# Kernel tuning notes

Hardware: AMD Instinct MI355X
Metric: run time of the kernel (lower is better)

The kernel has to match this reference:

```python
import jax, jax.numpy as jnp
import numpy as np

N_NODES = 100000
N_EDGES = 1600000
IN_C, HID_C, OUT_C = 128, 256, 128


def setup_inputs() -> dict:
    key = jax.random.key(0)
    ks = jax.random.split(key, 6)
    x = jax.random.normal(ks[0], (N_NODES, IN_C), dtype=jnp.float32)
    edge_index = jax.random.randint(ks[1], (2, N_EDGES), 0, N_NODES, dtype=jnp.int64)
    s = 0.05
    W1a = jax.random.normal(ks[2], (IN_C, HID_C), dtype=jnp.float32) * s
    b1a = jnp.zeros((HID_C,), dtype=jnp.float32)
    W2a = jax.random.normal(ks[3], (HID_C, HID_C), dtype=jnp.float32) * s
    b2a = jnp.zeros((HID_C,), dtype=jnp.float32)
    W1b = jax.random.normal(ks[4], (HID_C, HID_C), dtype=jnp.float32) * s
    b1b = jnp.zeros((HID_C,), dtype=jnp.float32)
    W2b = jax.random.normal(ks[5], (HID_C, OUT_C), dtype=jnp.float32) * s
    b2b = jnp.zeros((OUT_C,), dtype=jnp.float32)
    return {"x": x, "edge_index": edge_index, "W1a": W1a, "b1a": b1a,
            "W2a": W2a, "b2a": b2a, "W1b": W1b, "b1b": b1b,
            "W2b": W2b, "b2b": b2b}


def _gin_conv(x, src, dst, W1, b1, W2, b2):
    # GINConv (eps=0): nn( x + sum_{j in N(i)} x_j )
    agg = jax.ops.segment_sum(x[src], dst, num_segments=N_NODES)  # [N, d]
    h = x + agg
    h = jnp.maximum(h @ W1 + b1, 0.0)
    return h @ W2 + b2


def reference(x, edge_index, W1a, b1a, W2a, b2a, W1b, b1b, W2b, b2b):
    src, dst = edge_index[0], edge_index[1]
    h = jnp.maximum(_gin_conv(x, src, dst, W1a, b1a, W2a, b2a), 0.0)  # relu(conv1)
    # dropout is identity in eval mode
    out = _gin_conv(h, src, dst, W1b, b1b, W2b, b2b)  # conv2
    return out
```

## Files before the change

### kernel.cpp

```cpp
#include <hip/hip_runtime.h>


#define N_NODES 100000
#define N_EDGES 1600000
#define NBUCK 13

typedef unsigned short ushort_t;
typedef short bf16x8 __attribute__((ext_vector_type(8)));
typedef float floatx4 __attribute__((ext_vector_type(4)));

static __device__ __forceinline__ ushort_t f2bf(float f) {
    unsigned u = __float_as_uint(f);
    u = (u + 0x7FFFu + ((u >> 16) & 1u)) >> 16;
    return (ushort_t)u;
}
static __device__ __forceinline__ float bf2f(ushort_t u) {
    return __uint_as_float(((unsigned)u) << 16);
}

__global__ __launch_bounds__(256) void cvt_all_kernel(
    const float* __restrict__ W1a, const float* __restrict__ W2a,
    const float* __restrict__ W1b, const float* __restrict__ W2b,
    ushort_t* __restrict__ wt1a, ushort_t* __restrict__ wt2a,
    ushort_t* __restrict__ wt1b, ushort_t* __restrict__ wt2b) {
    int i = blockIdx.x * 256 + threadIdx.x;
    if (i < 32768) {
        int k = i >> 8, n = i & 255;
        wt1a[n * 128 + k] = f2bf(W1a[i]);
    } else if (i < 98304) {
        int j = i - 32768, k = j >> 8, n = j & 255;
        wt2a[n * 256 + k] = f2bf(W2a[j]);
    } else if (i < 163840) {
        int j = i - 98304, k = j >> 8, n = j & 255;
        wt1b[n * 256 + k] = f2bf(W1b[j]);
    } else if (i < 196608) {
        int j = i - 163840, k = j >> 7, n = j & 127;
        wt2b[n * 256 + k] = f2bf(W2b[j]);
    }
}

__global__ __launch_bounds__(256) void hist_kernel(const int* __restrict__ src,
                                                   const int* __restrict__ dst,
                                                   int* __restrict__ deg, int nE) {
    const int bucket = blockIdx.y;
    for (int e = blockIdx.x * 256 + threadIdx.x; e < nE; e += gridDim.x * 256) {
        int d = dst[e];
        int s = src[e];
        if ((unsigned)d < (unsigned)N_NODES && (unsigned)s < (unsigned)N_NODES &&
            (d >> 13) == bucket)
            atomicAdd(&deg[d], 1);
    }
}

__global__ __launch_bounds__(256) void fill_kernel(const int* __restrict__ src,
                                                   const int* __restrict__ dst,
                                                   int* __restrict__ cursor,
                                                   int* __restrict__ csr_src, int nE) {
    const int bucket = blockIdx.y;
    for (int e = blockIdx.x * 256 + threadIdx.x; e < nE; e += gridDim.x * 256) {
        int d = dst[e];
        int s = src[e];
        if ((unsigned)d < (unsigned)N_NODES && (unsigned)s < (unsigned)N_NODES &&
            (d >> 13) == bucket) {
            int pos = atomicAdd(&cursor[d], 1);
            csr_src[pos] = s;
        }
    }
}

__global__ __launch_bounds__(256) void scan1_kernel(const int* __restrict__ deg,
                                                    int* __restrict__ bsum, int n) {
    __shared__ int l[256];
    int b = blockIdx.x, t = threadIdx.x;
    int base = b * 1024 + t * 4;
    int s = 0;
#pragma unroll
    for (int k = 0; k < 4; ++k) {
        int i = base + k;
        if (i < n) s += deg[i];
    }
    l[t] = s;
    __syncthreads();
    for (int off = 128; off > 0; off >>= 1) {
        if (t < off) l[t] += l[t + off];
        __syncthreads();
    }
    if (t == 0) bsum[b] = l[0];
}

__global__ __launch_bounds__(128) void scan2_kernel(const int* __restrict__ bsum,
                                                    int* __restrict__ boff, int nb) {
    __shared__ int l[128];
    int t = threadIdx.x;
    int v = (t < nb) ? bsum[t] : 0;
    l[t] = v;
    __syncthreads();
    for (int off = 1; off < 128; off <<= 1) {
        int add = (t >= off) ? l[t - off] : 0;
        __syncthreads();
        l[t] += add;
        __syncthreads();
    }
    if (t < nb) boff[t] = l[t] - v;
}

__global__ __launch_bounds__(256) void scan3_kernel(const int* __restrict__ deg,
                                                    const int* __restrict__ boff,
                                                    int* __restrict__ row_ptr,
                                                    int* __restrict__ cursor, int n) {
    __shared__ int l[256];
    int b = blockIdx.x, t = threadIdx.x;
    int base = b * 1024 + t * 4;
    int d[4];
    int s = 0;
#pragma unroll
    for (int k = 0; k < 4; ++k) {
        int i = base + k;
        d[k] = (i < n) ? deg[i] : 0;
        s += d[k];
    }
    l[t] = s;
    __syncthreads();
    for (int off = 1; off < 256; off <<= 1) {
        int add = (t >= off) ? l[t - off] : 0;
        __syncthreads();
        l[t] += add;
        __syncthreads();
    }
    int run = boff[b] + l[t] - s;
#pragma unroll
    for (int k = 0; k < 4; ++k) {
        int i = base + k;
        if (i < n) {
            row_ptr[i] = run;
            cursor[i] = run;
        }
        run += d[k];
    }
}

template <int C, typename XT>
__global__ __launch_bounds__(256) void agg_gather_kernel(
    const XT* __restrict__ X, ushort_t* __restrict__ T,
    const int* __restrict__ row_ptr, const int* __restrict__ deg,
    const int* __restrict__ csr_src, int nN) {
    constexpr int VF = 8 / sizeof(XT);
    static_assert(64 * VF == C, "lane coverage must equal row width");
    const int lane = threadIdx.x & 63;
    const int wid = threadIdx.x >> 6;
    const int node = blockIdx.x * 4 + wid;
    if (node >= nN) return;

    float acc[VF];
    {
        const XT* row = X + (size_t)node * C + lane * VF;
        if constexpr (sizeof(XT) == 4) {
            float2 v = *(const float2*)row;
            acc[0] = v.x; acc[1] = v.y;
        } else {
            ushort4 u = *(const ushort4*)row;
            acc[0] = bf2f(u.x); acc[1] = bf2f(u.y);
            acc[2] = bf2f(u.z); acc[3] = bf2f(u.w);
        }
    }

    const int base = row_ptr[node];
    const int dg = deg[node];
    for (int j0 = 0; j0 < dg; j0 += 64) {
        int cnt = dg - j0;
        if (cnt > 64) cnt = 64;
        int nidx = (lane < cnt) ? csr_src[base + j0 + lane] : 0;
        if ((unsigned)nidx >= (unsigned)N_NODES) nidx = 0;
        int j = 0;
        for (; j + 3 < cnt; j += 4) {
            int s0 = __shfl(nidx, j);
            int s1 = __shfl(nidx, j + 1);
            int s2 = __shfl(nidx, j + 2);
            int s3 = __shfl(nidx, j + 3);
            if constexpr (sizeof(XT) == 4) {
                float2 v0 = *(const float2*)(X + (size_t)s0 * C + lane * VF);
                float2 v1 = *(const float2*)(X + (size_t)s1 * C + lane * VF);
                float2 v2 = *(const float2*)(X + (size_t)s2 * C + lane * VF);
                float2 v3 = *(const float2*)(X + (size_t)s3 * C + lane * VF);
                acc[0] += v0.x + v1.x + v2.x + v3.x;
                acc[1] += v0.y + v1.y + v2.y + v3.y;
            } else {
                ushort4 u0 = *(const ushort4*)(X + (size_t)s0 * C + lane * VF);
                ushort4 u1 = *(const ushort4*)(X + (size_t)s1 * C + lane * VF);
                ushort4 u2 = *(const ushort4*)(X + (size_t)s2 * C + lane * VF);
                ushort4 u3 = *(const ushort4*)(X + (size_t)s3 * C + lane * VF);
                acc[0] += bf2f(u0.x) + bf2f(u1.x) + bf2f(u2.x) + bf2f(u3.x);
                acc[1] += bf2f(u0.y) + bf2f(u1.y) + bf2f(u2.y) + bf2f(u3.y);
                acc[2] += bf2f(u0.z) + bf2f(u1.z) + bf2f(u2.z) + bf2f(u3.z);
                acc[3] += bf2f(u0.w) + bf2f(u1.w) + bf2f(u2.w) + bf2f(u3.w);
            }
        }
        for (; j < cnt; ++j) {
            int s0 = __shfl(nidx, j);
            if constexpr (sizeof(XT) == 4) {
                float2 v0 = *(const float2*)(X + (size_t)s0 * C + lane * VF);
                acc[0] += v0.x; acc[1] += v0.y;
            } else {
                ushort4 u0 = *(const ushort4*)(X + (size_t)s0 * C + lane * VF);
                acc[0] += bf2f(u0.x); acc[1] += bf2f(u0.y);
                acc[2] += bf2f(u0.z); acc[3] += bf2f(u0.w);
            }
        }
    }

    ushort_t* o = T + (size_t)node * C + lane * VF;
    if constexpr (VF == 2) {
        ushort2 w;
        w.x = f2bf(acc[0]); w.y = f2bf(acc[1]);
        *(ushort2*)o = w;
    } else {
        ushort4 w;
        w.x = f2bf(acc[0]); w.y = f2bf(acc[1]);
        w.z = f2bf(acc[2]); w.w = f2bf(acc[3]);
        *(ushort4*)o = w;
    }
}

template <bool RELU, typename OT>
__global__ __launch_bounds__(256) void gemm_kernel(
    const ushort_t* A, const ushort_t* __restrict__ Wt,
    const float* __restrict__ bias, OT* C, int M, int N, int K) {
    constexpr int BM = 128, BN = 128, BK = 32;
    constexpr int LDW = BK + 8;
    __shared__ ushort_t As[BM * LDW];
    __shared__ ushort_t Bs[BN * LDW];

    const int tid = threadIdx.x;
    const int lane = tid & 63;
    const int wid = tid >> 6;
    const int wm = wid & 1;
    const int wn = wid >> 1;
    const int l15 = lane & 15;
    const int q = lane >> 4;

    const int bm = blockIdx.x * BM;
    const int bn = blockIdx.y * BN;

    floatx4 acc[4][4];
#pragma unroll
    for (int mi = 0; mi < 4; ++mi)
#pragma unroll
        for (int ni = 0; ni < 4; ++ni) {
            floatx4 z = {0.f, 0.f, 0.f, 0.f};
            acc[mi][ni] = z;
        }

    for (int kt = 0; kt < K; kt += BK) {
#pragma unroll
        for (int p = 0; p < 4; ++p) {
            int i = p * 256 + tid;
            int row = i >> 3;
            int c4 = i & 7;
            int gr = bm + row;
            if (gr > M - 1) gr = M - 1;
            ushort4 u = *(const ushort4*)(A + (size_t)gr * K + kt + c4 * 4);
            *(ushort4*)&As[row * LDW + c4 * 4] = u;
        }
#pragma unroll
        for (int p = 0; p < 4; ++p) {
            int i = p * 256 + tid;
            int row = i >> 3;
            int c4 = i & 7;
            ushort4 u = *(const ushort4*)(Wt + (size_t)(bn + row) * K + kt + c4 * 4);
            *(ushort4*)&Bs[row * LDW + c4 * 4] = u;
        }
        __syncthreads();

        bf16x8 av[4], bv[4];
#pragma unroll
        for (int mi = 0; mi < 4; ++mi)
            av[mi] = *(const bf16x8*)&As[(wm * 64 + mi * 16 + l15) * LDW + q * 8];
#pragma unroll
        for (int ni = 0; ni < 4; ++ni)
            bv[ni] = *(const bf16x8*)&Bs[(wn * 64 + ni * 16 + l15) * LDW + q * 8];
#pragma unroll
        for (int mi = 0; mi < 4; ++mi)
#pragma unroll
            for (int ni = 0; ni < 4; ++ni)
                acc[mi][ni] = __builtin_amdgcn_mfma_f32_16x16x32_bf16(
                    av[mi], bv[ni], acc[mi][ni], 0, 0, 0);
        __syncthreads();
    }

    float bval[4];
#pragma unroll
    for (int ni = 0; ni < 4; ++ni) bval[ni] = bias[bn + wn * 64 + ni * 16 + l15];
#pragma unroll
    for (int mi = 0; mi < 4; ++mi) {
#pragma unroll
        for (int r = 0; r < 4; ++r) {
            int row = bm + wm * 64 + mi * 16 + q * 4 + r;
            if (row < M) {
#pragma unroll
                for (int ni = 0; ni < 4; ++ni) {
                    int col = bn + wn * 64 + ni * 16 + l15;
                    float v = acc[mi][ni][r] + bval[ni];
                    if (RELU) v = v > 0.f ? v : 0.f;
                    if constexpr (sizeof(OT) == 2)
                        C[(size_t)row * N + col] = f2bf(v);
                    else
                        C[(size_t)row * N + col] = v;
                }
            }
        }
    }
}

extern "C" void kernel_launch(void* const* d_in, const int* in_sizes, int n_in,
                              void* d_out, int out_size, void* d_ws, size_t ws_size,
                              hipStream_t stream) {
    const float* x   = (const float*)d_in[0];
    const int*   ei  = (const int*)d_in[1];
    const float* W1a = (const float*)d_in[2];
    const float* b1a = (const float*)d_in[3];
    const float* W2a = (const float*)d_in[4];
    const float* b2a = (const float*)d_in[5];
    const float* W1b = (const float*)d_in[6];
    const float* b1b = (const float*)d_in[7];
    const float* W2b = (const float*)d_in[8];
    const float* b2b = (const float*)d_in[9];
    const int* src = ei;
    const int* dst = ei + N_EDGES;
    float* out = (float*)d_out;

    char* base = (char*)d_ws;
    size_t o = 0;
    ushort_t* wt1a = (ushort_t*)(base + o); o += 128 * 256 * 2;
    ushort_t* wt2a = (ushort_t*)(base + o); o += 256 * 256 * 2;
    ushort_t* wt1b = (ushort_t*)(base + o); o += 256 * 256 * 2;
    ushort_t* wt2b = (ushort_t*)(base + o); o += 256 * 128 * 2;
    o = (o + 255) & ~(size_t)255;
    int* deg     = (int*)(base + o); o += (size_t)N_NODES * 4;
    int* row_ptr = (int*)(base + o); o += (size_t)N_NODES * 4;
    int* cursor  = (int*)(base + o); o += (size_t)N_NODES * 4;
    int* bsum    = (int*)(base + o); o += 128 * 4;
    int* boff    = (int*)(base + o); o += 128 * 4;
    o = (o + 255) & ~(size_t)255;
    int* csr_src = (int*)(base + o); o += (size_t)N_EDGES * 4;
    o = (o + 255) & ~(size_t)255;
    ushort_t* t1   = (ushort_t*)(base + o); o += (size_t)N_NODES * 128 * 2;
    ushort_t* tbig = (ushort_t*)(base + o); o += (size_t)N_NODES * 256 * 2;
    (void)ws_size; (void)o; (void)in_sizes; (void)n_in; (void)out_size;

    ushort_t* inter = (ushort_t*)d_out;

    cvt_all_kernel<<<768, 256, 0, stream>>>(W1a, W2a, W1b, W2b,
                                            wt1a, wt2a, wt1b, wt2b);

    const int NB = (N_NODES + 1023) / 1024;
    hipMemsetAsync(deg, 0, (size_t)N_NODES * 4, stream);
    hist_kernel<<<dim3(1024, NBUCK), 256, 0, stream>>>(src, dst, deg, N_EDGES);
    scan1_kernel<<<NB, 256, 0, stream>>>(deg, bsum, N_NODES);
    scan2_kernel<<<1, 128, 0, stream>>>(bsum, boff, NB);
    scan3_kernel<<<NB, 256, 0, stream>>>(deg, boff, row_ptr, cursor, N_NODES);
    fill_kernel<<<dim3(1024, NBUCK), 256, 0, stream>>>(src, dst, cursor, csr_src,
                                                       N_EDGES);

    const int gm = (N_NODES + 127) / 128;
    const int ga = (N_NODES + 3) / 4;

    agg_gather_kernel<128, float><<<ga, 256, 0, stream>>>(x, t1, row_ptr, deg,
                                                          csr_src, N_NODES);
    gemm_kernel<true, ushort_t><<<dim3(gm, 2), 256, 0, stream>>>(
        t1, wt1a, b1a, tbig, N_NODES, 256, 128);
    gemm_kernel<true, ushort_t><<<dim3(gm, 2), 256, 0, stream>>>(
        tbig, wt2a, b2a, inter, N_NODES, 256, 256);

    agg_gather_kernel<256, ushort_t><<<ga, 256, 0, stream>>>(inter, tbig, row_ptr,
                                                             deg, csr_src, N_NODES);
    gemm_kernel<true, ushort_t><<<dim3(gm, 2), 256, 0, stream>>>(
        tbig, wt1b, b1b, inter, N_NODES, 256, 256);
    gemm_kernel<false, float><<<dim3(gm, 1), 256, 0, stream>>>(
        inter, wt2b, b2b, out, N_NODES, 128, 256);
}
```

Before: 626.4 us.

## Convert x to bf16 and gather neighbor rows with 16-byte loads per lane

Adds a kernel that converts the fp32 input features to bf16 into the output buffer, so the first aggregation gathers half the bytes. The gather kernel is restructured so each lane loads 16 bytes (8 bf16) and several neighbors are processed in parallel across sub-groups of the wavefront, followed by a shuffle-xor reduction. This aims to raise memory-level parallelism and load width in the bandwidth-bound sparse aggregation. It costs an extra conversion pass, an in-wave reduction, and bf16 rounding of the layer-1 input.

Result: faster. 590.8 us (-5.7%).

```diff
diff --git a/kernel.cpp b/kernel.cpp
--- a/kernel.cpp
+++ b/kernel.cpp
@@ -14,8 +14,34 @@
     u = (u + 0x7FFFu + ((u >> 16) & 1u)) >> 16;
     return (ushort_t)u;
 }
-static __device__ __forceinline__ float bf2f(ushort_t u) {
-    return __uint_as_float(((unsigned)u) << 16);
+static __device__ __forceinline__ unsigned pack2bf(float lo, float hi) {
+    return (unsigned)f2bf(lo) | ((unsigned)f2bf(hi) << 16);
+}
+static __device__ __forceinline__ void addu4(float* acc, const uint4 v) {
+    const unsigned w0 = v.x, w1 = v.y, w2 = v.z, w3 = v.w;
+    acc[0] += __uint_as_float(w0 << 16);
+    acc[1] += __uint_as_float(w0 & 0xFFFF0000u);
+    acc[2] += __uint_as_float(w1 << 16);
+    acc[3] += __uint_as_float(w1 & 0xFFFF0000u);
+    acc[4] += __uint_as_float(w2 << 16);
+    acc[5] += __uint_as_float(w2 & 0xFFFF0000u);
+    acc[6] += __uint_as_float(w3 << 16);
+    acc[7] += __uint_as_float(w3 & 0xFFFF0000u);
+}
+
+__global__ __launch_bounds__(256) void cvt_x_kernel(const float* __restrict__ X,
+                                                    ushort_t* __restrict__ Xb, int n8) {
+    int i = blockIdx.x * 256 + threadIdx.x;
+    if (i < n8) {
+        const float4 a = ((const float4*)X)[2 * i];
+        const float4 b = ((const float4*)X)[2 * i + 1];
+        uint4 r;
+        r.x = pack2bf(a.x, a.y);
+        r.y = pack2bf(a.z, a.w);
+        r.z = pack2bf(b.x, b.y);
+        r.w = pack2bf(b.z, b.w);
+        ((uint4*)Xb)[i] = r;
+    }
 }
 
 __global__ __launch_bounds__(256) void cvt_all_kernel(
@@ -139,85 +165,69 @@
     }
 }
 
-template <int C, typename XT>
+template <int C>
 __global__ __launch_bounds__(256) void agg_gather_kernel(
-    const XT* __restrict__ X, ushort_t* __restrict__ T,
+    const ushort_t* __restrict__ X, ushort_t* __restrict__ T,
     const int* __restrict__ row_ptr, const int* __restrict__ deg,
     const int* __restrict__ csr_src, int nN) {
-    constexpr int VF = 8 / sizeof(XT);
-    static_assert(64 * VF == C, "lane coverage must equal row width");
+    constexpr int G = C / 8;
+    constexpr int NPW = 64 / G;
     const int lane = threadIdx.x & 63;
     const int wid = threadIdx.x >> 6;
     const int node = blockIdx.x * 4 + wid;
     if (node >= nN) return;
-
-    float acc[VF];
-    {
-        const XT* row = X + (size_t)node * C + lane * VF;
-        if constexpr (sizeof(XT) == 4) {
-            float2 v = *(const float2*)row;
-            acc[0] = v.x; acc[1] = v.y;
-        } else {
-            ushort4 u = *(const ushort4*)row;
-            acc[0] = bf2f(u.x); acc[1] = bf2f(u.y);
-            acc[2] = bf2f(u.z); acc[3] = bf2f(u.w);
-        }
-    }
+    const int sub = lane / G;
+    const size_t coff = (size_t)(lane % G) * 8;
+
+    float acc[8];
+#pragma unroll
+    for (int k = 0; k < 8; ++k) acc[k] = 0.f;
 
     const int base = row_ptr[node];
     const int dg = deg[node];
     for (int j0 = 0; j0 < dg; j0 += 64) {
         int cnt = dg - j0;
         if (cnt > 64) cnt = 64;
-        int nidx = (lane < cnt) ? csr_src[base + j0 + lane] : 0;
+        int nidx = 0;
+        if (lane < cnt) nidx = csr_src[base + j0 + lane];
         if ((unsigned)nidx >= (unsigned)N_NODES) nidx = 0;
         int j = 0;
-        for (; j + 3 < cnt; j += 4) {
-            int s0 = __shfl(nidx, j);
-            int s1 = __shfl(nidx, j + 1);
-            int s2 = __shfl(nidx, j + 2);
-            int s3 = __shfl(nidx, j + 3);
-            if constexpr (sizeof(XT) == 4) {
-                float2 v0 = *(const float2*)(X + (size_t)s0 * C + lane * VF);
-                float2 v1 = *(const float2*)(X + (size_t)s1 * C + lane * VF);
-                float2 v2 = *(const float2*)(X + (size_t)s2 * C + lane * VF);
-                float2 v3 = *(const float2*)(X + (size_t)s3 * C + lane * VF);
-                acc[0] += v0.x + v1.x + v2.x + v3.x;
-                acc[1] += v0.y + v1.y + v2.y + v3.y;
-            } else {
-                ushort4 u0 = *(const ushort4*)(X + (size_t)s0 * C + lane * VF);
-                ushort4 u1 = *(const ushort4*)(X + (size_t)s1 * C + lane * VF);
-                ushort4 u2 = *(const ushort4*)(X + (size_t)s2 * C + lane * VF);
-                ushort4 u3 = *(const ushort4*)(X + (size_t)s3 * C + lane * VF);
-                acc[0] += bf2f(u0.x) + bf2f(u1.x) + bf2f(u2.x) + bf2f(u3.x);
-                acc[1] += bf2f(u0.y) + bf2f(u1.y) + bf2f(u2.y) + bf2f(u3.y);
-                acc[2] += bf2f(u0.z) + bf2f(u1.z) + bf2f(u2.z) + bf2f(u3.z);
-                acc[3] += bf2f(u0.w) + bf2f(u1.w) + bf2f(u2.w) + bf2f(u3.w);
+        for (; j + 4 * NPW <= cnt; j += 4 * NPW) {
+            uint4 v[4];
+#pragma unroll
+            for (int u = 0; u < 4; ++u) {
+                int idx = __shfl(nidx, j + u * NPW + sub);
+                v[u] = *(const uint4*)(X + (size_t)idx * C + coff);
             }
-        }
-        for (; j < cnt; ++j) {
-            int s0 = __shfl(nidx, j);
-            if constexpr (sizeof(XT) == 4) {
-                float2 v0 = *(const float2*)(X + (size_t)s0 * C + lane * VF);
-                acc[0] += v0.x; acc[1] += v0.y;
-            } else {
-                ushort4 u0 = *(const ushort4*)(X + (size_t)s0 * C + lane * VF);
-                acc[0] += bf2f(u0.x); acc[1] += bf2f(u0.y);
-                acc[2] += bf2f(u0.z); acc[3] += bf2f(u0.w);
+#pragma unroll
+            for (int u = 0; u < 4; ++u) addu4(acc, v[u]);
+        }
+        for (; j < cnt; j += NPW) {
+            int jj = j + sub;
+            int srcl = (jj < cnt) ? jj : (cnt - 1);
+            int idx = __shfl(nidx, srcl);
+            if (jj < cnt) {
+                uint4 v = *(const uint4*)(X + (size_t)idx * C + coff);
+                addu4(acc, v);
             }
         }
     }
-
-    ushort_t* o = T + (size_t)node * C + lane * VF;
-    if constexpr (VF == 2) {
-        ushort2 w;
-        w.x = f2bf(acc[0]); w.y = f2bf(acc[1]);
-        *(ushort2*)o = w;
-    } else {
-        ushort4 w;
-        w.x = f2bf(acc[0]); w.y = f2bf(acc[1]);
-        w.z = f2bf(acc[2]); w.w = f2bf(acc[3]);
-        *(ushort4*)o = w;
+    if (sub == 0) {
+        uint4 v = *(const uint4*)(X + (size_t)node * C + coff);
+        addu4(acc, v);
+    }
+#pragma unroll
+    for (int off = G; off < 64; off <<= 1)
+#pragma unroll
+        for (int k = 0; k < 8; ++k) acc[k] += __shfl_xor(acc[k], off);
+
+    if (lane < G) {
+        uint4 r;
+        r.x = pack2bf(acc[0], acc[1]);
+        r.y = pack2bf(acc[2], acc[3]);
+        r.z = pack2bf(acc[4], acc[5]);
+        r.w = pack2bf(acc[6], acc[7]);
+        *(uint4*)(T + (size_t)node * C + coff) = r;
     }
 }
 
@@ -348,9 +358,12 @@
     (void)ws_size; (void)o; (void)in_sizes; (void)n_in; (void)out_size;
 
     ushort_t* inter = (ushort_t*)d_out;
+    ushort_t* xb    = (ushort_t*)d_out;
 
     cvt_all_kernel<<<768, 256, 0, stream>>>(W1a, W2a, W1b, W2b,
                                             wt1a, wt2a, wt1b, wt2b);
+    cvt_x_kernel<<<(N_NODES * 128 / 8 + 255) / 256, 256, 0, stream>>>(
+        x, xb, N_NODES * 128 / 8);
 
     const int NB = (N_NODES + 1023) / 1024;
     hipMemsetAsync(deg, 0, (size_t)N_NODES * 4, stream);
@@ -364,15 +377,15 @@
     const int gm = (N_NODES + 127) / 128;
     const int ga = (N_NODES + 3) / 4;
 
-    agg_gather_kernel<128, float><<<ga, 256, 0, stream>>>(x, t1, row_ptr, deg,
-                                                          csr_src, N_NODES);
+    agg_gather_kernel<128><<<ga, 256, 0, stream>>>(xb, t1, row_ptr, deg,
+                                                   csr_src, N_NODES);
     gemm_kernel<true, ushort_t><<<dim3(gm, 2), 256, 0, stream>>>(
         t1, wt1a, b1a, tbig, N_NODES, 256, 128);
     gemm_kernel<true, ushort_t><<<dim3(gm, 2), 256, 0, stream>>>(
         tbig, wt2a, b2a, inter, N_NODES, 256, 256);
 
-    agg_gather_kernel<256, ushort_t><<<ga, 256, 0, stream>>>(inter, tbig, row_ptr,
-                                                             deg, csr_src, N_NODES);
+    agg_gather_kernel<256><<<ga, 256, 0, stream>>>(inter, tbig, row_ptr,
+                                                   deg, csr_src, N_NODES);
     gemm_kernel<true, ushort_t><<<dim3(gm, 2), 256, 0, stream>>>(
         tbig, wt1b, b1b, inter, N_NODES, 256, 256);
     gemm_kernel<false, float><<<dim3(gm, 1), 256, 0, stream>>>(
```
